# Optimization experiments

Hardware: AMD Instinct MI355X
Metric: run time of the kernel (lower is better)

The kernel has to match this reference:

```python
import jax, jax.numpy as jnp
import numpy as np

B, LQ, LK = 8, 1024, 1024
QD, KD, VD, OD, H = 512, 256, 256, 512, 8
HD = OD // H
SCALE = float(np.sqrt(HD))


def setup_inputs() -> dict:
    key = jax.random.key(0)
    ks = jax.random.split(key, 11)
    def lin(k, fan_in, fan_out):
        bound = 1.0 / np.sqrt(fan_in)
        kw, kb = jax.random.split(k)
        W = jax.random.uniform(kw, (fan_in, fan_out), jnp.float32, -bound, bound)
        b = jax.random.uniform(kb, (fan_out,), jnp.float32, -bound, bound)
        return W, b
    Wq, bq = lin(ks[0], QD, OD)
    Wk, bk = lin(ks[1], KD, OD)
    Wv, bv = lin(ks[2], VD, OD)
    Wo, bo = lin(ks[3], OD, OD)
    return {
        "query": jax.random.normal(ks[4], (B, LQ, QD), jnp.float32),
        "key": jax.random.normal(ks[5], (B, LK, KD), jnp.float32),
        "value": jax.random.normal(ks[6], (B, LK, VD), jnp.float32),
        "Wq": Wq, "bq": bq, "Wk": Wk, "bk": bk,
        "Wv": Wv, "bv": bv, "Wo": Wo, "bo": bo,
    }


def reference(query, key, value, Wq, bq, Wk, bk, Wv, bv, Wo, bo):
    b = query.shape[0]
    # project and split heads: (B, H, L, HD)
    q = (query @ Wq + bq).reshape(b, -1, H, HD).transpose(0, 2, 1, 3)
    k = (key @ Wk + bk).reshape(b, -1, H, HD).transpose(0, 2, 1, 3)
    v = (value @ Wv + bv).reshape(b, -1, H, HD).transpose(0, 2, 1, 3)
    scores = jnp.einsum("bhqd,bhkd->bhqk", q, k) / SCALE
    attention = jax.nn.softmax(scores, axis=-1)
    # dropout is identity in eval mode (reference uses eval semantics)
    out = jnp.einsum("bhqk,bhkd->bhqd", attention, v)
    out = out.transpose(0, 2, 1, 3).reshape(b, -1, H * HD)
    out = out @ Wo + bo
    return out, attention
```

## Files before the change

kernel.cpp:

```cpp
#include <hip/hip_runtime.h>

typedef __attribute__((ext_vector_type(8))) short s8b;
typedef __attribute__((ext_vector_type(4))) float f32x4;

#define MFMA_BF16(a, b, c) __builtin_amdgcn_mfma_f32_16x16x32_bf16((a), (b), (c), 0, 0, 0)

__device__ __forceinline__ short f2bf(float f) {
    unsigned u = __float_as_uint(f);
    u += 0x7fffu + ((u >> 16) & 1u);
    return (short)(u >> 16);
}

template <int OMODE, bool ABF16>
__global__ __launch_bounds__(256) void gemm_k(const void* __restrict__ Ain,
                                              const float* __restrict__ W,
                                              const float* __restrict__ bias,
                                              void* __restrict__ Cout,
                                              int K, float scale) {
    __shared__ short As[128][40];
    __shared__ short Bs[128][40];

    const int tid  = threadIdx.x;
    const int lane = tid & 63;
    const int wid  = tid >> 6;
    const int l15  = lane & 15, lhi = lane >> 4;
    const int wr   = wid >> 1, wc = wid & 1;
    const int bm   = blockIdx.x << 7;
    const int bn   = blockIdx.y << 7;

    const f32x4 zf = {0.f, 0.f, 0.f, 0.f};
    f32x4 acc[4][4];
#pragma unroll
    for (int i = 0; i < 4; ++i)
#pragma unroll
        for (int j = 0; j < 4; ++j) acc[i][j] = zf;

    const int arow = tid >> 1;
    const int ak0  = (tid & 1) << 4;
    const int bn_t = tid & 127;
    const int bk0  = (tid >> 7) << 4;

    const int nkt = K >> 5;
    for (int kt = 0; kt < nkt; ++kt) {
        __syncthreads();
        if (ABF16) {
            const short* src = (const short*)Ain + (size_t)(bm + arow) * K + (kt << 5) + ak0;
            *(s8b*)&As[arow][ak0]     = *(const s8b*)(src);
            *(s8b*)&As[arow][ak0 + 8] = *(const s8b*)(src + 8);
        } else {
            const float* src = (const float*)Ain + (size_t)(bm + arow) * K + (kt << 5) + ak0;
            s8b t0, t1;
#pragma unroll
            for (int i = 0; i < 8; ++i) { t0[i] = f2bf(src[i]); t1[i] = f2bf(src[i + 8]); }
            *(s8b*)&As[arow][ak0]     = t0;
            *(s8b*)&As[arow][ak0 + 8] = t1;
        }
        {
            s8b t0, t1;
#pragma unroll
            for (int j = 0; j < 8; ++j)
                t0[j] = f2bf(W[(size_t)((kt << 5) + bk0 + j) * 512 + bn + bn_t]);
#pragma unroll
            for (int j = 0; j < 8; ++j)
                t1[j] = f2bf(W[(size_t)((kt << 5) + bk0 + 8 + j) * 512 + bn + bn_t]);
            *(s8b*)&Bs[bn_t][bk0]     = t0;
            *(s8b*)&Bs[bn_t][bk0 + 8] = t1;
        }
        __syncthreads();
        s8b a[4], b[4];
#pragma unroll
        for (int rt = 0; rt < 4; ++rt)
            a[rt] = *(const s8b*)&As[(wr << 6) + (rt << 4) + l15][lhi << 3];
#pragma unroll
        for (int ct = 0; ct < 4; ++ct)
            b[ct] = *(const s8b*)&Bs[(wc << 6) + (ct << 4) + l15][lhi << 3];
#pragma unroll
        for (int rt = 0; rt < 4; ++rt)
#pragma unroll
            for (int ct = 0; ct < 4; ++ct)
                acc[rt][ct] = MFMA_BF16(a[rt], b[ct], acc[rt][ct]);
    }

#pragma unroll
    for (int rt = 0; rt < 4; ++rt)
#pragma unroll
        for (int ct = 0; ct < 4; ++ct) {
            const int col  = bn + (wc << 6) + (ct << 4) + l15;
            const float bv = bias[col];
#pragma unroll
            for (int r = 0; r < 4; ++r) {
                const int row = bm + (wr << 6) + (rt << 4) + (lhi << 2) + r;
                const float v = (acc[rt][ct][r] + bv) * scale;
                if (OMODE == 0) {
                    ((short*)Cout)[(size_t)row * 512 + col] = f2bf(v);
                } else if (OMODE == 1) {
                    const int bb = row >> 10, kv = row & 1023;
                    ((short*)Cout)[((size_t)(bb * 512 + col) << 10) + kv] = f2bf(v);
                } else {
                    ((float*)Cout)[(size_t)row * 512 + col] = v;
                }
            }
        }
}

__global__ __launch_bounds__(256) void attn_k(const short* __restrict__ Qp,
                                              const short* __restrict__ Kp,
                                              const short* __restrict__ Vt,
                                              float* __restrict__ attn,
                                              short* __restrict__ Oint) {
    __shared__ short Plds[4][32][72];

    const int tid = threadIdx.x;
    const int wid = tid >> 6, lane = tid & 63;
    const int l15 = lane & 15, lhi = lane >> 4;
    const int bid = blockIdx.x;
    const int qc = bid & 7, h = (bid >> 3) & 7, b = bid >> 6;
    const int q0 = (qc << 7) + (wid << 5);

    const size_t qbase = ((size_t)(b * 1024 + q0)) * 512 + h * 64;
    s8b aq[2][2];
#pragma unroll
    for (int rt = 0; rt < 2; ++rt)
#pragma unroll
        for (int ks = 0; ks < 2; ++ks)
            aq[rt][ks] = *(const s8b*)&Qp[qbase + (size_t)((rt << 4) + l15) * 512 + (ks << 5) + (lhi << 3)];

    float m8[8], l8[8];
#pragma unroll
    for (int i = 0; i < 8; ++i) { m8[i] = -1e30f; l8[i] = 0.f; }

    const size_t kbase = ((size_t)(b * 1024)) * 512 + h * 64;

    for (int kt = 0; kt < 16; ++kt) {
        s8b bk[4][2];
#pragma unroll
        for (int c = 0; c < 4; ++c)
#pragma unroll
            for (int ks = 0; ks < 2; ++ks)
                bk[c][ks] = *(const s8b*)&Kp[kbase + (size_t)((kt << 6) + (c << 4) + l15) * 512 + (ks << 5) + (lhi << 3)];
        const f32x4 zf = {0.f, 0.f, 0.f, 0.f};
        f32x4 s[2][4];
#pragma unroll
        for (int rt = 0; rt < 2; ++rt)
#pragma unroll
            for (int c = 0; c < 4; ++c) {
                s[rt][c] = zf;
                s[rt][c] = MFMA_BF16(aq[rt][0], bk[c][0], s[rt][c]);
                s[rt][c] = MFMA_BF16(aq[rt][1], bk[c][1], s[rt][c]);
            }
#pragma unroll
        for (int rt = 0; rt < 2; ++rt)
#pragma unroll
            for (int r = 0; r < 4; ++r) {
                const int idx = (rt << 2) + r;
                const float v0 = s[rt][0][r], v1 = s[rt][1][r];
                const float v2 = s[rt][2][r], v3 = s[rt][3][r];
                const float vm = fmaxf(fmaxf(v0, v1), fmaxf(v2, v3));
                const float mn = fmaxf(m8[idx], vm);
                const float corr = exp2f(m8[idx] - mn);
                const float add = exp2f(v0 - mn) + exp2f(v1 - mn) + exp2f(v2 - mn) + exp2f(v3 - mn);
                l8[idx] = l8[idx] * corr + add;
                m8[idx] = mn;
            }
    }
#pragma unroll
    for (int i = 0; i < 8; ++i) {
        float m = m8[i], l = l8[i];
#pragma unroll
        for (int mask = 1; mask <= 8; mask <<= 1) {
            const float mo = __shfl_xor(m, mask, 64);
            const float lo = __shfl_xor(l, mask, 64);
            const float mn = fmaxf(m, mo);
            l = l * exp2f(m - mn) + lo * exp2f(mo - mn);
            m = mn;
        }
        m8[i] = m;
        l8[i] = 1.0f / l;
    }

    const f32x4 zf = {0.f, 0.f, 0.f, 0.f};
    f32x4 o[2][4];
#pragma unroll
    for (int rt = 0; rt < 2; ++rt)
#pragma unroll
        for (int cd = 0; cd < 4; ++cd) o[rt][cd] = zf;

    const size_t vbase = ((size_t)(((b << 3) + h) << 6)) << 10;
    const size_t abase = ((size_t)(((b << 3) + h) * 1024 + q0)) << 10;

    for (int kt = 0; kt < 16; ++kt) {
        s8b bk[4][2];
#pragma unroll
        for (int c = 0; c < 4; ++c)
#pragma unroll
            for (int ks = 0; ks < 2; ++ks)
                bk[c][ks] = *(const s8b*)&Kp[kbase + (size_t)((kt << 6) + (c << 4) + l15) * 512 + (ks << 5) + (lhi << 3)];
        f32x4 s[2][4];
#pragma unroll
        for (int rt = 0; rt < 2; ++rt)
#pragma unroll
            for (int c = 0; c < 4; ++c) {
                s[rt][c] = zf;
                s[rt][c] = MFMA_BF16(aq[rt][0], bk[c][0], s[rt][c]);
                s[rt][c] = MFMA_BF16(aq[rt][1], bk[c][1], s[rt][c]);
            }
#pragma unroll
        for (int rt = 0; rt < 2; ++rt)
#pragma unroll
            for (int c = 0; c < 4; ++c)
#pragma unroll
                for (int r = 0; r < 4; ++r) {
                    const int idx = (rt << 2) + r;
                    s[rt][c][r] = exp2f(s[rt][c][r] - m8[idx]) * l8[idx];
                }
#pragma unroll
        for (int rt = 0; rt < 2; ++rt)
#pragma unroll
            for (int r = 0; r < 4; ++r) {
                const int prow = (rt << 4) + (lhi << 2) + r;
                const size_t ar = abase + ((size_t)prow << 10) + (kt << 6);
#pragma unroll
                for (int c = 0; c < 4; ++c) {
                    attn[ar + (c << 4) + l15] = s[rt][c][r];
                    Plds[wid][prow][(c << 4) + l15] = f2bf(s[rt][c][r]);
                }
            }
        s8b pa[2][2], bv[4][2];
#pragma unroll
        for (int rt = 0; rt < 2; ++rt)
#pragma unroll
            for (int ks = 0; ks < 2; ++ks)
                pa[rt][ks] = *(const s8b*)&Plds[wid][(rt << 4) + l15][(ks << 5) + (lhi << 3)];
#pragma unroll
        for (int cd = 0; cd < 4; ++cd)
#pragma unroll
            for (int ks = 0; ks < 2; ++ks)
                bv[cd][ks] = *(const s8b*)&Vt[vbase + (size_t)((cd << 4) + l15) * 1024 + (kt << 6) + (ks << 5) + (lhi << 3)];
#pragma unroll
        for (int rt = 0; rt < 2; ++rt)
#pragma unroll
            for (int cd = 0; cd < 4; ++cd) {
                o[rt][cd] = MFMA_BF16(pa[rt][0], bv[cd][0], o[rt][cd]);
                o[rt][cd] = MFMA_BF16(pa[rt][1], bv[cd][1], o[rt][cd]);
            }
    }

#pragma unroll
    for (int rt = 0; rt < 2; ++rt)
#pragma unroll
        for (int cd = 0; cd < 4; ++cd)
#pragma unroll
            for (int r = 0; r < 4; ++r) {
                const size_t orow =
                    ((size_t)(b * 1024 + q0 + (rt << 4) + (lhi << 2) + r)) * 512 + h * 64 + (cd << 4) + l15;
                Oint[orow] = f2bf(o[rt][cd][r]);
            }
}

extern "C" void kernel_launch(void* const* d_in, const int* in_sizes, int n_in,
                              void* d_out, int out_size, void* d_ws, size_t ws_size,
                              hipStream_t stream) {
    (void)in_sizes; (void)n_in; (void)out_size; (void)ws_size;

    const float* query = (const float*)d_in[0];
    const float* key   = (const float*)d_in[1];
    const float* value = (const float*)d_in[2];
    const float* Wq = (const float*)d_in[3];
    const float* bq = (const float*)d_in[4];
    const float* Wk = (const float*)d_in[5];
    const float* bk = (const float*)d_in[6];
    const float* Wv = (const float*)d_in[7];
    const float* bv = (const float*)d_in[8];
    const float* Wo = (const float*)d_in[9];
    const float* bo = (const float*)d_in[10];

    float* out  = (float*)d_out;
    float* attn = out + (size_t)8 * 1024 * 512;

    char* ws    = (char*)d_ws;
    short* Qp   = (short*)(ws);
    short* Kp   = (short*)(ws + (8u << 20));
    short* Vt   = (short*)(ws + (16u << 20));
    short* Oint = (short*)(ws + (24u << 20));

    const dim3 blk(256);
    const dim3 gg(64, 4);
    const float qscale = 0.18033688011112042f;

    gemm_k<0, false><<<gg, blk, 0, stream>>>(query, Wq, bq, Qp, 512, qscale);
    gemm_k<0, false><<<gg, blk, 0, stream>>>(key,   Wk, bk, Kp, 256, 1.0f);
    gemm_k<1, false><<<gg, blk, 0, stream>>>(value, Wv, bv, Vt, 256, 1.0f);
    attn_k<<<dim3(512), blk, 0, stream>>>(Qp, Kp, Vt, attn, Oint);
    gemm_k<2, true><<<gg, blk, 0, stream>>>(Oint, Wo, bo, out, 512, 1.0f);
}
```

Measured before the change: 463.1 us.

## Halve attention rows per wave and add separate LDS-based V transpose kernel

The attention kernel now gives each wave 16 query rows instead of 32, doubling the grid to 1024 blocks to raise occupancy and parallelism. The cost is that each K and V tile is loaded twice as often per query. The V projection GEMM now writes row-major output, and a new kernel transposes it through shared memory with vectorized stores. This replaces the strided 2-byte scattered transposed writes in the GEMM epilogue, at the price of an extra launch and a round trip through memory.

```diff
diff --git a/kernel.cpp b/kernel.cpp
--- a/kernel.cpp
+++ b/kernel.cpp
@@ -93,14 +93,38 @@
                 const float v = (acc[rt][ct][r] + bv) * scale;
                 if (OMODE == 0) {
                     ((short*)Cout)[(size_t)row * 512 + col] = f2bf(v);
-                } else if (OMODE == 1) {
-                    const int bb = row >> 10, kv = row & 1023;
-                    ((short*)Cout)[((size_t)(bb * 512 + col) << 10) + kv] = f2bf(v);
                 } else {
                     ((float*)Cout)[(size_t)row * 512 + col] = v;
                 }
             }
         }
+}
+
+__global__ __launch_bounds__(256) void vtrans_k(const short* __restrict__ Vp,
+                                                short* __restrict__ Vt) {
+    __shared__ short Vs[64][72];
+
+    const int tid = threadIdx.x;
+    const int bid = blockIdx.x;
+    const int kvt = bid & 15, h = (bid >> 4) & 7, b = bid >> 7;
+    const int kv0 = kvt << 6;
+
+    const int r  = tid >> 2;
+    const int c0 = (tid & 3) << 4;
+    const short* src = Vp + (size_t)(b * 1024 + kv0 + r) * 512 + h * 64 + c0;
+    const s8b v0 = *(const s8b*)(src);
+    const s8b v1 = *(const s8b*)(src + 8);
+#pragma unroll
+    for (int i = 0; i < 8; ++i) Vs[c0 + i][r] = v0[i];
+#pragma unroll
+    for (int i = 0; i < 8; ++i) Vs[c0 + 8 + i][r] = v1[i];
+    __syncthreads();
+
+    const int d  = tid >> 2;
+    const int k0 = (tid & 3) << 4;
+    short* dst = Vt + ((size_t)(((b << 3) + h) << 6) + d) * 1024 + kv0 + k0;
+    *(s8b*)dst       = *(const s8b*)&Vs[d][k0];
+    *(s8b*)(dst + 8) = *(const s8b*)&Vs[d][k0 + 8];
 }
 
 __global__ __launch_bounds__(256) void attn_k(const short* __restrict__ Qp,
@@ -108,28 +132,27 @@
                                               const short* __restrict__ Vt,
                                               float* __restrict__ attn,
                                               short* __restrict__ Oint) {
-    __shared__ short Plds[4][32][72];
+    __shared__ short Plds[4][16][72];
 
     const int tid = threadIdx.x;
     const int wid = tid >> 6, lane = tid & 63;
     const int l15 = lane & 15, lhi = lane >> 4;
     const int bid = blockIdx.x;
-    const int qc = bid & 7, h = (bid >> 3) & 7, b = bid >> 6;
-    const int q0 = (qc << 7) + (wid << 5);
+    const int qc = bid & 15, h = (bid >> 4) & 7, b = bid >> 7;
+    const int q0 = (qc << 6) + (wid << 4);
 
     const size_t qbase = ((size_t)(b * 1024 + q0)) * 512 + h * 64;
-    s8b aq[2][2];
-#pragma unroll
-    for (int rt = 0; rt < 2; ++rt)
-#pragma unroll
-        for (int ks = 0; ks < 2; ++ks)
-            aq[rt][ks] = *(const s8b*)&Qp[qbase + (size_t)((rt << 4) + l15) * 512 + (ks << 5) + (lhi << 3)];
-
-    float m8[8], l8[8];
-#pragma unroll
-    for (int i = 0; i < 8; ++i) { m8[i] = -1e30f; l8[i] = 0.f; }
+    s8b aq[2];
+#pragma unroll
+    for (int ks = 0; ks < 2; ++ks)
+        aq[ks] = *(const s8b*)&Qp[qbase + (size_t)l15 * 512 + (ks << 5) + (lhi << 3)];
+
+    float m8[4], l8[4];
+#pragma unroll
+    for (int i = 0; i < 4; ++i) { m8[i] = -1e30f; l8[i] = 0.f; }
 
     const size_t kbase = ((size_t)(b * 1024)) * 512 + h * 64;
+    const f32x4 zf = {0.f, 0.f, 0.f, 0.f};
 
     for (int kt = 0; kt < 16; ++kt) {
         s8b bk[4][2];
@@ -138,33 +161,27 @@
 #pragma unroll
             for (int ks = 0; ks < 2; ++ks)
                 bk[c][ks] = *(const s8b*)&Kp[kbase + (size_t)((kt << 6) + (c << 4) + l15) * 512 + (ks << 5) + (lhi << 3)];
-        const f32x4 zf = {0.f, 0.f, 0.f, 0.f};
-        f32x4 s[2][4];
-#pragma unroll
-        for (int rt = 0; rt < 2; ++rt)
-#pragma unroll
-            for (int c = 0; c < 4; ++c) {
-                s[rt][c] = zf;
-                s[rt][c] = MFMA_BF16(aq[rt][0], bk[c][0], s[rt][c]);
-                s[rt][c] = MFMA_BF16(aq[rt][1], bk[c][1], s[rt][c]);
-            }
-#pragma unroll
-        for (int rt = 0; rt < 2; ++rt)
-#pragma unroll
-            for (int r = 0; r < 4; ++r) {
-                const int idx = (rt << 2) + r;
-                const float v0 = s[rt][0][r], v1 = s[rt][1][r];
-                const float v2 = s[rt][2][r], v3 = s[rt][3][r];
-                const float vm = fmaxf(fmaxf(v0, v1), fmaxf(v2, v3));
-                const float mn = fmaxf(m8[idx], vm);
-                const float corr = exp2f(m8[idx] - mn);
-                const float add = exp2f(v0 - mn) + exp2f(v1 - mn) + exp2f(v2 - mn) + exp2f(v3 - mn);
-                l8[idx] = l8[idx] * corr + add;
-                m8[idx] = mn;
-            }
-    }
-#pragma unroll
-    for (int i = 0; i < 8; ++i) {
+        f32x4 s[4];
+#pragma unroll
+        for (int c = 0; c < 4; ++c) {
+            s[c] = zf;
+            s[c] = MFMA_BF16(aq[0], bk[c][0], s[c]);
+            s[c] = MFMA_BF16(aq[1], bk[c][1], s[c]);
+        }
+#pragma unroll
+        for (int r = 0; r < 4; ++r) {
+            const float v0 = s[0][r], v1 = s[1][r];
+            const float v2 = s[2][r], v3 = s[3][r];
+            const float vm = fmaxf(fmaxf(v0, v1), fmaxf(v2, v3));
+            const float mn = fmaxf(m8[r], vm);
+            const float corr = exp2f(m8[r] - mn);
+            const float add = exp2f(v0 - mn) + exp2f(v1 - mn) + exp2f(v2 - mn) + exp2f(v3 - mn);
+            l8[r] = l8[r] * corr + add;
+            m8[r] = mn;
+        }
+    }
+#pragma unroll
+    for (int i = 0; i < 4; ++i) {
         float m = m8[i], l = l8[i];
 #pragma unroll
         for (int mask = 1; mask <= 8; mask <<= 1) {
@@ -178,12 +195,9 @@
         l8[i] = 1.0f / l;
     }
 
-    const f32x4 zf = {0.f, 0.f, 0.f, 0.f};
-    f32x4 o[2][4];
-#pragma unroll
-    for (int rt = 0; rt < 2; ++rt)
-#pragma unroll
-        for (int cd = 0; cd < 4; ++cd) o[rt][cd] = zf;
+    f32x4 o[4];
+#pragma unroll
+    for (int cd = 0; cd < 4; ++cd) o[cd] = zf;
 
     const size_t vbase = ((size_t)(((b << 3) + h) << 6)) << 10;
     const size_t abase = ((size_t)(((b << 3) + h) * 1024 + q0)) << 10;
@@ -195,66 +209,52 @@
 #pragma unroll
             for (int ks = 0; ks < 2; ++ks)
                 bk[c][ks] = *(const s8b*)&Kp[kbase + (size_t)((kt << 6) + (c << 4) + l15) * 512 + (ks << 5) + (lhi << 3)];
-        f32x4 s[2][4];
-#pragma unroll
-        for (int rt = 0; rt < 2; ++rt)
+        f32x4 s[4];
+#pragma unroll
+        for (int c = 0; c < 4; ++c) {
+            s[c] = zf;
+            s[c] = MFMA_BF16(aq[0], bk[c][0], s[c]);
+            s[c] = MFMA_BF16(aq[1], bk[c][1], s[c]);
+        }
+#pragma unroll
+        for (int c = 0; c < 4; ++c)
+#pragma unroll
+            for (int r = 0; r < 4; ++r)
+                s[c][r] = exp2f(s[c][r] - m8[r]) * l8[r];
+#pragma unroll
+        for (int r = 0; r < 4; ++r) {
+            const int prow = (lhi << 2) + r;
+            const size_t ar = abase + ((size_t)prow << 10) + (kt << 6);
 #pragma unroll
             for (int c = 0; c < 4; ++c) {
-                s[rt][c] = zf;
-                s[rt][c] = MFMA_BF16(aq[rt][0], bk[c][0], s[rt][c]);
-                s[rt][c] = MFMA_BF16(aq[rt][1], bk[c][1], s[rt][c]);
+                attn[ar + (c << 4) + l15] = s[c][r];
+                Plds[wid][prow][(c << 4) + l15] = f2bf(s[c][r]);
             }
-#pragma unroll
-        for (int rt = 0; rt < 2; ++rt)
-#pragma unroll
-            for (int c = 0; c < 4; ++c)
-#pragma unroll
-                for (int r = 0; r < 4; ++r) {
-                    const int idx = (rt << 2) + r;
-                    s[rt][c][r] = exp2f(s[rt][c][r] - m8[idx]) * l8[idx];
-                }
-#pragma unroll
-        for (int rt = 0; rt < 2; ++rt)
-#pragma unroll
-            for (int r = 0; r < 4; ++r) {
-                const int prow = (rt << 4) + (lhi << 2) + r;
-                const size_t ar = abase + ((size_t)prow << 10) + (kt << 6);
-#pragma unroll
-                for (int c = 0; c < 4; ++c) {
-                    attn[ar + (c << 4) + l15] = s[rt][c][r];
-                    Plds[wid][prow][(c << 4) + l15] = f2bf(s[rt][c][r]);
-                }
-            }
-        s8b pa[2][2], bv[4][2];
-#pragma unroll
-        for (int rt = 0; rt < 2; ++rt)
-#pragma unroll
-            for (int ks = 0; ks < 2; ++ks)
-                pa[rt][ks] = *(const s8b*)&Plds[wid][(rt << 4) + l15][(ks << 5) + (lhi << 3)];
+        }
+        s8b pa[2], bv[4][2];
+#pragma unroll
+        for (int ks = 0; ks < 2; ++ks)
+            pa[ks] = *(const s8b*)&Plds[wid][l15][(ks << 5) + (lhi << 3)];
 #pragma unroll
         for (int cd = 0; cd < 4; ++cd)
 #pragma unroll
             for (int ks = 0; ks < 2; ++ks)
                 bv[cd][ks] = *(const s8b*)&Vt[vbase + (size_t)((cd << 4) + l15) * 1024 + (kt << 6) + (ks << 5) + (lhi << 3)];
 #pragma unroll
-        for (int rt = 0; rt < 2; ++rt)
-#pragma unroll
-            for (int cd = 0; cd < 4; ++cd) {
-                o[rt][cd] = MFMA_BF16(pa[rt][0], bv[cd][0], o[rt][cd]);
-                o[rt][cd] = MFMA_BF16(pa[rt][1], bv[cd][1], o[rt][cd]);
-            }
-    }
-
-#pragma unroll
-    for (int rt = 0; rt < 2; ++rt)
-#pragma unroll
-        for (int cd = 0; cd < 4; ++cd)
-#pragma unroll
-            for (int r = 0; r < 4; ++r) {
-                const size_t orow =
-                    ((size_t)(b * 1024 + q0 + (rt << 4) + (lhi << 2) + r)) * 512 + h * 64 + (cd << 4) + l15;
-                Oint[orow] = f2bf(o[rt][cd][r]);
-            }
+        for (int cd = 0; cd < 4; ++cd) {
+            o[cd] = MFMA_BF16(pa[0], bv[cd][0], o[cd]);
+            o[cd] = MFMA_BF16(pa[1], bv[cd][1], o[cd]);
+        }
+    }
+
+#pragma unroll
+    for (int cd = 0; cd < 4; ++cd)
+#pragma unroll
+        for (int r = 0; r < 4; ++r) {
+            const size_t orow =
+                ((size_t)(b * 1024 + q0 + (lhi << 2) + r)) * 512 + h * 64 + (cd << 4) + l15;
+            Oint[orow] = f2bf(o[cd][r]);
+        }
 }
 
 extern "C" void kernel_launch(void* const* d_in, const int* in_sizes, int n_in,
@@ -280,8 +280,9 @@
     char* ws    = (char*)d_ws;
     short* Qp   = (short*)(ws);
     short* Kp   = (short*)(ws + (8u << 20));
-    short* Vt   = (short*)(ws + (16u << 20));
-    short* Oint = (short*)(ws + (24u << 20));
+    short* Vp   = (short*)(ws + (16u << 20));
+    short* Vt   = (short*)(ws + (24u << 20));
+    short* Oint = (short*)(ws + (32u << 20));
 
     const dim3 blk(256);
     const dim3 gg(64, 4);
@@ -289,7 +290,8 @@
 
     gemm_k<0, false><<<gg, blk, 0, stream>>>(query, Wq, bq, Qp, 512, qscale);
     gemm_k<0, false><<<gg, blk, 0, stream>>>(key,   Wk, bk, Kp, 256, 1.0f);
-    gemm_k<1, false><<<gg, blk, 0, stream>>>(value, Wv, bv, Vt, 256, 1.0f);
-    attn_k<<<dim3(512), blk, 0, stream>>>(Qp, Kp, Vt, attn, Oint);
+    gemm_k<0, false><<<gg, blk, 0, stream>>>(value, Wv, bv, Vp, 256, 1.0f);
+    vtrans_k<<<dim3(1024), blk, 0, stream>>>(Vp, Vt);
+    attn_k<<<dim3(1024), blk, 0, stream>>>(Qp, Kp, Vt, attn, Oint);
     gemm_k<2, true><<<gg, blk, 0, stream>>>(Oint, Wo, bo, out, 512, 1.0f);
 }
```

Result: slower. 541.1 us (+16.9%).
